# Optimization experiments

Hardware: AMD Instinct MI355X
Metric: run time of the kernel (lower is better)

The kernel has to match this reference:

```python
import jax, jax.numpy as jnp
import numpy as np


def _conv(x, w, b):
    # 3x3 stride-1 pad-1 conv, NCHW / OIHW
    y = jax.lax.conv_general_dilated(x, w, (1, 1), 'SAME',
                                     dimension_numbers=('NCHW', 'OIHW', 'NCHW'))
    return y + b[None, :, None, None]


def _lrelu(x):
    return jax.nn.leaky_relu(x, negative_slope=0.2)


def setup_inputs() -> dict:
    key = jax.random.key(0)
    ks = jax.random.split(key, 12)
    B, H, W = 64, 32, 32
    C, K, DH, OUT = 16, 10, 256, 784

    def w(k, shape, fan_in):
        return jax.random.normal(k, shape, jnp.float32) / np.sqrt(fan_in)

    inp = {
        'x':   jax.random.normal(ks[0], (B, 1, H, W), jnp.float32),
        # encoder convs
        'cw1': w(ks[1], (C, 1, 3, 3), 1 * 9),   'cb1': jnp.zeros((C,), jnp.float32),
        'cw2': w(ks[2], (C, C, 3, 3), C * 9),   'cb2': jnp.zeros((C,), jnp.float32),
        # 2 residual blocks, 2 convs each
        'r1w1': w(ks[3], (C, C, 3, 3), C * 9), 'r1b1': jnp.zeros((C,), jnp.float32),
        'r1w2': w(ks[4], (C, C, 3, 3), C * 9), 'r1b2': jnp.zeros((C,), jnp.float32),
        'r2w1': w(ks[5], (C, C, 3, 3), C * 9), 'r2b1': jnp.zeros((C,), jnp.float32),
        'r2w2': w(ks[6], (C, C, 3, 3), C * 9), 'r2b2': jnp.zeros((C,), jnp.float32),
        # VQ codebook (k=10 hardcoded in source, d = encoder channels)
        'codebook': jax.random.normal(ks[7], (K, C), jnp.float32),
        # decoder MLP 16 -> 256 -> 256 -> 784 (torch Linear layout: [out, in])
        'dw1': w(ks[8], (DH, C), C),     'db1': jnp.zeros((DH,), jnp.float32),
        'dw2': w(ks[9], (DH, DH), DH),   'db2': jnp.zeros((DH,), jnp.float32),
        'dw3': w(ks[10], (OUT, DH), DH), 'db3': jnp.zeros((OUT,), jnp.float32),
    }
    return inp


def reference(x, cw1, cb1, cw2, cb2,
              r1w1, r1b1, r1w2, r1b2, r2w1, r2b1, r2w2, r2b2,
              codebook, dw1, db1, dw2, db2, dw3, db3):
    # ---- encoder ----
    h = _lrelu(_conv(x, cw1, cb1))
    h = _lrelu(_conv(h, cw2, cb2))
    h = _lrelu(_conv(_lrelu(_conv(h, r1w1, r1b1)), r1w2, r1b2)) + h  # ResBlock 1
    h = _lrelu(_conv(_lrelu(_conv(h, r2w1, r2b1)), r2w2, r2b2)) + h  # ResBlock 2
    z_e = h  # [B, C, H, W]

    # ---- VQ: cdist^2 + argmin + gather ----
    B, C, H, W = z_e.shape
    x_flat = z_e.transpose(0, 2, 3, 1).reshape(-1, C)          # [N, C]
    d2 = (jnp.sum(x_flat ** 2, axis=1, keepdims=True)
          + jnp.sum(codebook ** 2, axis=1)[None, :]
          - 2.0 * x_flat @ codebook.T)                          # [N, K]
    idx = jnp.argmin(d2, axis=1)                                # [N]
    z_q = codebook[idx].reshape(B, H, W, C).transpose(0, 3, 1, 2)
    # straight-through (as written in source: value == z_e, grad flows via z_q)
    z_st = z_q + jax.lax.stop_gradient(z_e - z_q)               # [B, C, H, W]

    # ---- decoder: per-pixel MLP 16 -> 256 -> 256 -> 784 ----
    g = z_st.transpose(0, 2, 3, 1)                              # [B, H, W, C]
    g = _lrelu(g @ dw1.T + db1)
    g = _lrelu(g @ dw2.T + db2)
    x_recon = jax.nn.sigmoid(g @ dw3.T + db3)                   # [B, H, W, 784]
    return x_recon, z_e, z_st, z_q
```

## Files before the change

kernel.cpp:

```cpp
#include <hip/hip_runtime.h>

typedef __attribute__((ext_vector_type(8))) short bfrag;
typedef __attribute__((ext_vector_type(4))) float ffrag;

__device__ __forceinline__ float lrelu(float x) { return x > 0.f ? x : 0.2f * x; }

__device__ __forceinline__ short f2b(float f) {
    union { float f; unsigned u; } x; x.f = f;
    unsigned r = x.u + 0x7fffu + ((x.u >> 16) & 1u);
    return (short)(r >> 16);
}

__global__ __launch_bounds__(256) void prep_k(
    const float* __restrict__ dw1, const float* __restrict__ dw2, const float* __restrict__ dw3,
    short* __restrict__ dw1p, short* __restrict__ dw2b, short* __restrict__ dw3b)
{
    const int i = blockIdx.x * 256 + threadIdx.x;
    if (i < 65536)  dw2b[i] = f2b(dw2[i]);
    if (i < 200704) dw3b[i] = f2b(dw3[i]);
    if (i < 8192) {
        const int row = i >> 5, k = i & 31;
        dw1p[i] = (k < 16) ? f2b(dw1[row * 16 + k]) : (short)0;
    }
}

template<int CIN, bool RES, bool VQ>
__global__ __launch_bounds__(256, 6) void conv3_k(
    const float* __restrict__ in, const float* __restrict__ wgt,
    const float* __restrict__ bias, const float* __restrict__ res,
    float* __restrict__ out,
    const float* __restrict__ cbk, float* __restrict__ zq,
    float* __restrict__ zst, short* __restrict__ zstb)
{
    __shared__ float sw[16 * CIN * 9];
    __shared__ float si[CIN][4][34];
    __shared__ float sx[VQ ? 64 * 17 : 1];
    __shared__ float scb[VQ ? 160 : 1];
    __shared__ int   sbest[VQ ? 64 : 1];

    const int t = threadIdx.x;
    const int b = blockIdx.x >> 4;
    const int band = blockIdx.x & 15;
    const float* ip = in + (size_t)b * CIN * 1024;

    for (int i = t; i < 16 * CIN * 9; i += 256) sw[i] = wgt[i];
    if (VQ) { if (t < 160) scb[t] = cbk[t]; }
    for (int i = t; i < CIN * 136; i += 256) {
        const int ci = i / 136;
        const int rem = i - ci * 136;
        const int rr = rem / 34;
        const int cc = rem - rr * 34;
        const int row = band * 2 + rr - 1;
        const int cv  = cc - 1;
        si[ci][rr][cc] = (row >= 0 && row < 32 && cv >= 0 && cv < 32)
                       ? ip[ci * 1024 + row * 32 + cv] : 0.f;
    }
    __syncthreads();

    const int w0 = (t & 15) * 2;
    const int rr = (t >> 4) & 1;
    const int co = (t >> 5) * 2;

    float acc[2][2];
    #pragma unroll
    for (int j = 0; j < 2; ++j) {
        const float bv = bias[co + j];
        acc[j][0] = bv; acc[j][1] = bv;
    }

    #pragma unroll
    for (int ci = 0; ci < CIN; ++ci)
        #pragma unroll
        for (int kh = 0; kh < 3; ++kh) {
            const float* srow = &si[ci][rr + kh][w0];
            float v[4];
            #pragma unroll
            for (int m = 0; m < 4; ++m) v[m] = srow[m];
            #pragma unroll
            for (int j = 0; j < 2; ++j) {
                const float* wp = &sw[((co + j) * CIN + ci) * 9 + kh * 3];
                #pragma unroll
                for (int kw = 0; kw < 3; ++kw) {
                    const float wv = wp[kw];
                    acc[j][0] = fmaf(v[kw],     wv, acc[j][0]);
                    acc[j][1] = fmaf(v[kw + 1], wv, acc[j][1]);
                }
            }
        }

    const int row = band * 2 + rr;
    #pragma unroll
    for (int j = 0; j < 2; ++j) {
        const size_t o = (size_t)b * 16384 + (size_t)(co + j) * 1024 + row * 32 + w0;
        float2 ov;
        ov.x = lrelu(acc[j][0]); ov.y = lrelu(acc[j][1]);
        if (RES) {
            const float2 rv = *(const float2*)&res[o];
            ov.x += rv.x; ov.y += rv.y;
        }
        *(float2*)&out[o] = ov;
        if (VQ) {
            sx[(rr * 32 + w0)     * 17 + co + j] = ov.x;
            sx[(rr * 32 + w0 + 1) * 17 + co + j] = ov.y;
        }
    }

    if (VQ) {
        __syncthreads();
        if (t < 64) {
            float x[16]; float xx = 0.f;
            #pragma unroll
            for (int c = 0; c < 16; ++c) { x[c] = sx[t * 17 + c]; xx += x[c] * x[c]; }
            int best = 0; float bestd = 1e30f;
            #pragma unroll
            for (int k = 0; k < 10; ++k) {
                float dot = 0.f, cn = 0.f;
                #pragma unroll
                for (int c = 0; c < 16; ++c) { const float cv = scb[k * 16 + c]; dot += x[c] * cv; cn += cv * cv; }
                const float d2 = xx + cn - 2.f * dot;
                if (d2 < bestd) { bestd = d2; best = k; }
            }
            sbest[t] = best;
            unsigned pk[8];
            #pragma unroll
            for (int c = 0; c < 16; ++c) {
                const float q = scb[best * 16 + c];
                const float s = q + (x[c] - q);
                const unsigned hb = (unsigned)(unsigned short)f2b(s);
                if (c & 1) pk[c >> 1] |= hb << 16; else pk[c >> 1] = hb;
            }
            const size_t n = (size_t)b * 1024 + (band * 2 + (t >> 5)) * 32 + (t & 31);
            uint4* d = (uint4*)(zstb + n * 16);
            d[0] = make_uint4(pk[0], pk[1], pk[2], pk[3]);
            d[1] = make_uint4(pk[4], pk[5], pk[6], pk[7]);
        }
        __syncthreads();
        for (int i = t; i < 1024; i += 256) {
            const int c  = i >> 6;
            const int rw = i & 63;
            const float q = scb[sbest[rw] * 16 + c];
            const float x = sx[rw * 17 + c];
            const size_t a = (size_t)b * 16384 + (size_t)c * 1024 + band * 64 + rw;
            zq[a]  = q;
            zst[a] = q + (x - q);
        }
    }
}

__global__ __launch_bounds__(256, 2) void decoder_k(
    const short* __restrict__ zstb,
    const short* __restrict__ dw1p, const float* __restrict__ db1,
    const short* __restrict__ dw2b, const float* __restrict__ db2,
    const short* __restrict__ dw3b, const float* __restrict__ db3,
    float* __restrict__ xrec)
{
    __shared__ short g[4 * 8192];
    __shared__ short b3[2][4096];

    const int t    = threadIdx.x;
    const int lane = t & 63;
    const int wid  = t >> 6;
    const int lr   = lane & 15;
    const int lg   = lane >> 4;
    const int row0 = blockIdx.x * 128 + wid * 32;
    short* gw = g + wid * 8192;

    #define GB(row, kbyte) (((row) * 512 + (kbyte)) ^ (((row) & 7) << 4))

    auto stage2 = [&](short* dst, const short* src) {
        #pragma unroll
        for (int h = 0; h < 2; ++h) {
            const int L = h * 4096 + t * 16;
            const int S = L ^ (((L >> 9) & 7) << 4);
            __builtin_amdgcn_global_load_lds(
                (const __attribute__((address_space(1))) void*)((const char*)src + S),
                (__attribute__((address_space(3))) void*)((char*)dst + L), 16, 0, 0);
        }
    };

    stage2(&b3[0][0], dw2b);

    {
        bfrag A1[2];
        #pragma unroll
        for (int rt = 0; rt < 2; ++rt) {
            bfrag z;
            #pragma unroll
            for (int i = 0; i < 8; ++i) z[i] = 0;
            if (lg < 2)
                z = *(const bfrag*)&zstb[(size_t)(row0 + rt * 16 + lr) * 16 + lg * 8];
            A1[rt] = z;
        }
        #pragma unroll
        for (int ct = 0; ct < 16; ++ct) {
            const int col = ct * 16 + lr;
            const bfrag B = *(const bfrag*)&dw1p[col * 32 + lg * 8];
            const float bv = db1[col];
            ffrag acc[2];
            #pragma unroll
            for (int rt = 0; rt < 2; ++rt) {
                #pragma unroll
                for (int q = 0; q < 4; ++q) acc[rt][q] = bv;
                acc[rt] = __builtin_amdgcn_mfma_f32_16x16x32_bf16(A1[rt], B, acc[rt], 0, 0, 0);
            }
            #pragma unroll
            for (int rt = 0; rt < 2; ++rt)
                #pragma unroll
                for (int q = 0; q < 4; ++q) {
                    const int R = rt * 16 + lg * 4 + q;
                    *(short*)((char*)gw + GB(R, col * 2)) = f2b(lrelu(acc[rt][q]));
                }
        }
    }

    bfrag A[2][8];
    #pragma unroll
    for (int rt = 0; rt < 2; ++rt)
        #pragma unroll
        for (int kk = 0; kk < 8; ++kk)
            A[rt][kk] = *(const bfrag*)((char*)gw + GB(rt * 16 + lr, kk * 64 + lg * 16));

    __syncthreads();

    #pragma unroll 1
    for (int p = 0; p < 16; ++p) {
        if (p < 15) stage2(&b3[(p + 1) & 1][0], dw2b + (p + 1) * 4096);
        else        stage2(&b3[0][0],           dw3b);
        const char* bp = (const char*)&b3[p & 1][0];
        const int col = p * 16 + lr;
        bfrag Bf[8];
        #pragma unroll
        for (int kk = 0; kk < 8; ++kk)
            Bf[kk] = *(const bfrag*)(bp + (((lr * 512 + kk * 64 + lg * 16)) ^ ((lr & 7) << 4)));
        ffrag aE[2], aO[2];
        const float bv = db2[col];
        #pragma unroll
        for (int rt = 0; rt < 2; ++rt)
            #pragma unroll
            for (int q = 0; q < 4; ++q) { aE[rt][q] = bv; aO[rt][q] = 0.f; }
        #pragma unroll
        for (int kk = 0; kk < 8; kk += 2)
            #pragma unroll
            for (int rt = 0; rt < 2; ++rt) {
                aE[rt] = __builtin_amdgcn_mfma_f32_16x16x32_bf16(A[rt][kk],     Bf[kk],     aE[rt], 0, 0, 0);
                aO[rt] = __builtin_amdgcn_mfma_f32_16x16x32_bf16(A[rt][kk + 1], Bf[kk + 1], aO[rt], 0, 0, 0);
            }
        #pragma unroll
        for (int rt = 0; rt < 2; ++rt)
            #pragma unroll
            for (int q = 0; q < 4; ++q) {
                const int R = rt * 16 + lg * 4 + q;
                *(short*)((char*)gw + GB(R, col * 2)) = f2b(lrelu(aE[rt][q] + aO[rt][q]));
            }
        __syncthreads();
    }

    #pragma unroll
    for (int rt = 0; rt < 2; ++rt)
        #pragma unroll
        for (int kk = 0; kk < 8; ++kk)
            A[rt][kk] = *(const bfrag*)((char*)gw + GB(rt * 16 + lr, kk * 64 + lg * 16));

    float* slab = (float*)gw;

    #pragma unroll 1
    for (int p = 0; p < 49; ++p) {
        if (p < 48) stage2(&b3[(p + 1) & 1][0], dw3b + (p + 1) * 4096);
        const char* bp = (const char*)&b3[p & 1][0];
        const int col = p * 16 + lr;
        bfrag Bf[8];
        #pragma unroll
        for (int kk = 0; kk < 8; ++kk)
            Bf[kk] = *(const bfrag*)(bp + (((lr * 512 + kk * 64 + lg * 16)) ^ ((lr & 7) << 4)));
        ffrag aE[2], aO[2];
        const float bv = db3[col];
        #pragma unroll
        for (int rt = 0; rt < 2; ++rt)
            #pragma unroll
            for (int q = 0; q < 4; ++q) { aE[rt][q] = bv; aO[rt][q] = 0.f; }
        #pragma unroll
        for (int kk = 0; kk < 8; kk += 2)
            #pragma unroll
            for (int rt = 0; rt < 2; ++rt) {
                aE[rt] = __builtin_amdgcn_mfma_f32_16x16x32_bf16(A[rt][kk],     Bf[kk],     aE[rt], 0, 0, 0);
                aO[rt] = __builtin_amdgcn_mfma_f32_16x16x32_bf16(A[rt][kk + 1], Bf[kk + 1], aO[rt], 0, 0, 0);
            }
        const int ph = p & 1;
        #pragma unroll
        for (int rt = 0; rt < 2; ++rt)
            #pragma unroll
            for (int q = 0; q < 4; ++q) {
                const int R = rt * 16 + lg * 4 + q;
                const float v = aE[rt][q] + aO[rt][q];
                slab[R * 36 + ph * 16 + lr] = 1.f / (1.f + __expf(-v));
            }
        if (ph) {
            const int cb = (p - 1) * 16;
            #pragma unroll
            for (int f0 = 0; f0 < 4; ++f0) {
                const int f = f0 * 64 + lane;
                const int row = f >> 3, c4 = f & 7;
                const float4 v = *(const float4*)&slab[row * 36 + c4 * 4];
                *(float4*)&xrec[(size_t)(row0 + row) * 784 + cb + c4 * 4] = v;
            }
        }
        if (p == 48) {
            #pragma unroll
            for (int f0 = 0; f0 < 2; ++f0) {
                const int f = f0 * 64 + lane;
                const int row = f >> 2, c4 = f & 3;
                const float4 v = *(const float4*)&slab[row * 36 + c4 * 4];
                *(float4*)&xrec[(size_t)(row0 + row) * 784 + 768 + c4 * 4] = v;
            }
        }
        __syncthreads();
    }
    #undef GB
}

extern "C" void kernel_launch(void* const* d_in, const int* in_sizes, int n_in,
                              void* d_out, int out_size, void* d_ws, size_t ws_size,
                              hipStream_t stream) {
    const float* x    = (const float*)d_in[0];
    const float* cw1  = (const float*)d_in[1];
    const float* cb1  = (const float*)d_in[2];
    const float* cw2  = (const float*)d_in[3];
    const float* cb2  = (const float*)d_in[4];
    const float* r1w1 = (const float*)d_in[5];
    const float* r1b1 = (const float*)d_in[6];
    const float* r1w2 = (const float*)d_in[7];
    const float* r1b2 = (const float*)d_in[8];
    const float* r2w1 = (const float*)d_in[9];
    const float* r2b1 = (const float*)d_in[10];
    const float* r2w2 = (const float*)d_in[11];
    const float* r2b2 = (const float*)d_in[12];
    const float* cbk  = (const float*)d_in[13];
    const float* dw1  = (const float*)d_in[14];
    const float* db1  = (const float*)d_in[15];
    const float* dw2  = (const float*)d_in[16];
    const float* db2  = (const float*)d_in[17];
    const float* dw3  = (const float*)d_in[18];
    const float* db3  = (const float*)d_in[19];

    float* out  = (float*)d_out;
    float* xrec = out;
    float* ze   = out + 51380224;
    float* zst  = ze + 1048576;
    float* zq   = zst + 1048576;

    float* A  = (float*)d_ws;
    float* Bf = A + (1 << 20);
    float* Cf = Bf + (1 << 20);
    short* wsb  = (short*)(Cf + (1 << 20));
    short* zstb = wsb;
    short* dw2b = zstb + 1048576;
    short* dw3b = dw2b + 65536;
    short* dw1p = dw3b + 200704;

    prep_k<<<784, 256, 0, stream>>>(dw1, dw2, dw3, dw1p, dw2b, dw3b);

    conv3_k<1,  false, false><<<1024, 256, 0, stream>>>(x,  cw1,  cb1,  nullptr, A,  nullptr, nullptr, nullptr, nullptr);
    conv3_k<16, false, false><<<1024, 256, 0, stream>>>(A,  cw2,  cb2,  nullptr, Bf, nullptr, nullptr, nullptr, nullptr);
    conv3_k<16, false, false><<<1024, 256, 0, stream>>>(Bf, r1w1, r1b1, nullptr, Cf, nullptr, nullptr, nullptr, nullptr);
    conv3_k<16, true,  false><<<1024, 256, 0, stream>>>(Cf, r1w2, r1b2, Bf, A,  nullptr, nullptr, nullptr, nullptr);
    conv3_k<16, false, false><<<1024, 256, 0, stream>>>(A,  r2w1, r2b1, nullptr, Cf, nullptr, nullptr, nullptr, nullptr);
    conv3_k<16, true,  true ><<<1024, 256, 0, stream>>>(Cf, r2w2, r2b2, A, ze, cbk, zq, zst, zstb);

    decoder_k<<<512, 256, 0, stream>>>(zstb, dw1p, db1, dw2b, db2, dw3b, db3, xrec);
}
```

Baseline: 169.0 us.

## Fuse six encoder convs and VQ into one halo-tiled kernel

```diff
diff --git a/kernel.cpp b/kernel.cpp
--- a/kernel.cpp
+++ b/kernel.cpp
@@ -13,7 +13,11 @@
 
 __global__ __launch_bounds__(256) void prep_k(
     const float* __restrict__ dw1, const float* __restrict__ dw2, const float* __restrict__ dw3,
-    short* __restrict__ dw1p, short* __restrict__ dw2b, short* __restrict__ dw3b)
+    const float* __restrict__ cw1, const float* __restrict__ cw2,
+    const float* __restrict__ r1w1, const float* __restrict__ r1w2,
+    const float* __restrict__ r2w1, const float* __restrict__ r2w2,
+    short* __restrict__ dw1p, short* __restrict__ dw2b, short* __restrict__ dw3b,
+    float* __restrict__ wtr)
 {
     const int i = blockIdx.x * 256 + threadIdx.x;
     if (i < 65536)  dw2b[i] = f2b(dw2[i]);
@@ -22,128 +26,153 @@
         const int row = i >> 5, k = i & 31;
         dw1p[i] = (k < 16) ? f2b(dw1[row * 16 + k]) : (short)0;
     }
-}
-
-template<int CIN, bool RES, bool VQ>
-__global__ __launch_bounds__(256, 6) void conv3_k(
-    const float* __restrict__ in, const float* __restrict__ wgt,
-    const float* __restrict__ bias, const float* __restrict__ res,
-    float* __restrict__ out,
-    const float* __restrict__ cbk, float* __restrict__ zq,
+    if (i < 2304) {
+        const int co = i & 15;
+        const int q  = i >> 4;
+        const int k  = q % 9;
+        const int ci = q / 9;
+        const int src = (co * 16 + ci) * 9 + k;
+        wtr[2304 * 1 + i] = cw2 [src];
+        wtr[2304 * 2 + i] = r1w1[src];
+        wtr[2304 * 3 + i] = r1w2[src];
+        wtr[2304 * 4 + i] = r2w1[src];
+        wtr[2304 * 5 + i] = r2w2[src];
+        if (ci == 0) wtr[i] = cw1[co * 9 + k];
+    }
+}
+
+template<int CIN, int RIN, int ROUT, int HOUT, bool HASRES, int RRES, int HRES>
+__device__ __forceinline__ void conv_stage(
+    const float* __restrict__ in, float* __restrict__ out, const float* __restrict__ res,
+    const float* __restrict__ wt, const float* __restrict__ bias, int r0, int t)
+{
+    const int lo = (r0 - HOUT > 0) ? r0 - HOUT : 0;
+    const int hi = (r0 + 8 + HOUT < 32) ? r0 + 8 + HOUT : 32;
+    const int base = r0 - HOUT;
+    const int nlow = lo - base;
+    const int hih  = hi - base;
+    if (nlow > 0 || hih < ROUT) {
+        const int nz = (nlow + (ROUT - hih)) * 36;
+        for (int i = t; i < 16 * nz; i += 512) {
+            const int ch = i / nz, rem = i % nz;
+            int r = rem / 36; const int c = rem % 36;
+            r = (r < nlow) ? r : (hih + (r - nlow));
+            out[(ch * ROUT + r) * 36 + c] = 0.f;
+        }
+    }
+    for (int i = t; i < 16 * ROUT * 2; i += 512) {
+        const int ch = i / (ROUT * 2), rem = i % (ROUT * 2);
+        out[(ch * ROUT + (rem >> 1)) * 36 + ((rem & 1) ? 33 : 0)] = 0.f;
+    }
+
+    const int n = (hi - lo) * 32;
+    for (int u = t; u < n; u += 512) {
+        const int row = lo + (u >> 5), col = u & 31;
+        const int prin = row - r0 + HOUT;
+        float acc[16];
+        #pragma unroll
+        for (int co = 0; co < 16; ++co) acc[co] = bias[co];
+        for (int ci = 0; ci < CIN; ++ci) {
+            const float* ip = in + (ci * RIN + prin) * 36 + col;
+            float v[9];
+            #pragma unroll
+            for (int kh = 0; kh < 3; ++kh)
+                #pragma unroll
+                for (int kw = 0; kw < 3; ++kw) v[kh * 3 + kw] = ip[kh * 36 + kw];
+            const float* wp = wt + ci * 144;
+            #pragma unroll
+            for (int k = 0; k < 9; ++k)
+                #pragma unroll
+                for (int co = 0; co < 16; ++co)
+                    acc[co] = fmaf(v[k], wp[k * 16 + co], acc[co]);
+        }
+        const int pro = row - base;
+        #pragma unroll
+        for (int co = 0; co < 16; ++co) {
+            float val = lrelu(acc[co]);
+            if (HASRES) val += res[(co * RRES + (row - (r0 - HRES))) * 36 + col + 1];
+            out[(co * ROUT + pro) * 36 + col + 1] = val;
+        }
+    }
+    __syncthreads();
+}
+
+__global__ __launch_bounds__(512, 1) void enc_k(
+    const float* __restrict__ x, const float* __restrict__ wtr,
+    const float* __restrict__ cb1, const float* __restrict__ cb2,
+    const float* __restrict__ r1b1, const float* __restrict__ r1b2,
+    const float* __restrict__ r2b1, const float* __restrict__ r2b2,
+    const float* __restrict__ cbk,
+    float* __restrict__ ze, float* __restrict__ zq,
     float* __restrict__ zst, short* __restrict__ zstb)
 {
-    __shared__ float sw[16 * CIN * 9];
-    __shared__ float si[CIN][4][34];
-    __shared__ float sx[VQ ? 64 * 17 : 1];
-    __shared__ float scb[VQ ? 160 : 1];
-    __shared__ int   sbest[VQ ? 64 : 1];
-
-    const int t = threadIdx.x;
-    const int b = blockIdx.x >> 4;
-    const int band = blockIdx.x & 15;
-    const float* ip = in + (size_t)b * CIN * 1024;
-
-    for (int i = t; i < 16 * CIN * 9; i += 256) sw[i] = wgt[i];
-    if (VQ) { if (t < 160) scb[t] = cbk[t]; }
-    for (int i = t; i < CIN * 136; i += 256) {
-        const int ci = i / 136;
-        const int rem = i - ci * 136;
-        const int rr = rem / 34;
-        const int cc = rem - rr * 34;
-        const int row = band * 2 + rr - 1;
-        const int cv  = cc - 1;
-        si[ci][rr][cc] = (row >= 0 && row < 32 && cv >= 0 && cv < 32)
-                       ? ip[ci * 1024 + row * 32 + cv] : 0.f;
+    __shared__ float xb[20 * 36];
+    __shared__ float Abuf[16 * 18 * 36];
+    __shared__ float Bbuf[16 * 16 * 36];
+    __shared__ float Cbuf[16 * 12 * 36];
+    __shared__ float scb[160];
+    __shared__ int   sbest[256];
+
+    const int t  = threadIdx.x;
+    const int b  = blockIdx.x >> 2;
+    const int r0 = (blockIdx.x & 3) * 8;
+
+    if (t < 160) scb[t] = cbk[t];
+    for (int i = t; i < 720; i += 512) {
+        const int r = i / 36, c = i % 36;
+        const int rl = r0 - 6 + r, cl = c - 1;
+        xb[i] = (rl >= 0 && rl < 32 && cl >= 0 && cl < 32)
+              ? x[(size_t)b * 1024 + rl * 32 + cl] : 0.f;
     }
     __syncthreads();
 
-    const int w0 = (t & 15) * 2;
-    const int rr = (t >> 4) & 1;
-    const int co = (t >> 5) * 2;
-
-    float acc[2][2];
-    #pragma unroll
-    for (int j = 0; j < 2; ++j) {
-        const float bv = bias[co + j];
-        acc[j][0] = bv; acc[j][1] = bv;
-    }
-
-    #pragma unroll
-    for (int ci = 0; ci < CIN; ++ci)
-        #pragma unroll
-        for (int kh = 0; kh < 3; ++kh) {
-            const float* srow = &si[ci][rr + kh][w0];
-            float v[4];
-            #pragma unroll
-            for (int m = 0; m < 4; ++m) v[m] = srow[m];
-            #pragma unroll
-            for (int j = 0; j < 2; ++j) {
-                const float* wp = &sw[((co + j) * CIN + ci) * 9 + kh * 3];
-                #pragma unroll
-                for (int kw = 0; kw < 3; ++kw) {
-                    const float wv = wp[kw];
-                    acc[j][0] = fmaf(v[kw],     wv, acc[j][0]);
-                    acc[j][1] = fmaf(v[kw + 1], wv, acc[j][1]);
-                }
-            }
-        }
-
-    const int row = band * 2 + rr;
-    #pragma unroll
-    for (int j = 0; j < 2; ++j) {
-        const size_t o = (size_t)b * 16384 + (size_t)(co + j) * 1024 + row * 32 + w0;
-        float2 ov;
-        ov.x = lrelu(acc[j][0]); ov.y = lrelu(acc[j][1]);
-        if (RES) {
-            const float2 rv = *(const float2*)&res[o];
-            ov.x += rv.x; ov.y += rv.y;
-        }
-        *(float2*)&out[o] = ov;
-        if (VQ) {
-            sx[(rr * 32 + w0)     * 17 + co + j] = ov.x;
-            sx[(rr * 32 + w0 + 1) * 17 + co + j] = ov.y;
-        }
-    }
-
-    if (VQ) {
-        __syncthreads();
-        if (t < 64) {
-            float x[16]; float xx = 0.f;
-            #pragma unroll
-            for (int c = 0; c < 16; ++c) { x[c] = sx[t * 17 + c]; xx += x[c] * x[c]; }
-            int best = 0; float bestd = 1e30f;
-            #pragma unroll
-            for (int k = 0; k < 10; ++k) {
-                float dot = 0.f, cn = 0.f;
-                #pragma unroll
-                for (int c = 0; c < 16; ++c) { const float cv = scb[k * 16 + c]; dot += x[c] * cv; cn += cv * cv; }
-                const float d2 = xx + cn - 2.f * dot;
-                if (d2 < bestd) { bestd = d2; best = k; }
-            }
-            sbest[t] = best;
-            unsigned pk[8];
-            #pragma unroll
-            for (int c = 0; c < 16; ++c) {
-                const float q = scb[best * 16 + c];
-                const float s = q + (x[c] - q);
-                const unsigned hb = (unsigned)(unsigned short)f2b(s);
-                if (c & 1) pk[c >> 1] |= hb << 16; else pk[c >> 1] = hb;
-            }
-            const size_t n = (size_t)b * 1024 + (band * 2 + (t >> 5)) * 32 + (t & 31);
-            uint4* d = (uint4*)(zstb + n * 16);
-            d[0] = make_uint4(pk[0], pk[1], pk[2], pk[3]);
-            d[1] = make_uint4(pk[4], pk[5], pk[6], pk[7]);
-        }
-        __syncthreads();
-        for (int i = t; i < 1024; i += 256) {
-            const int c  = i >> 6;
-            const int rw = i & 63;
-            const float q = scb[sbest[rw] * 16 + c];
-            const float x = sx[rw * 17 + c];
-            const size_t a = (size_t)b * 16384 + (size_t)c * 1024 + band * 64 + rw;
-            zq[a]  = q;
-            zst[a] = q + (x - q);
-        }
+    conv_stage<1,  20, 18, 5, false,  1, 0>(xb,   Abuf, nullptr, wtr,          cb1,  r0, t);
+    conv_stage<16, 18, 16, 4, false,  1, 0>(Abuf, Bbuf, nullptr, wtr + 2304,   cb2,  r0, t);
+    conv_stage<16, 16, 14, 3, false,  1, 0>(Bbuf, Abuf, nullptr, wtr + 4608,   r1b1, r0, t);
+    conv_stage<16, 14, 12, 2, true,  16, 4>(Abuf, Cbuf, Bbuf,    wtr + 6912,   r1b2, r0, t);
+    conv_stage<16, 12, 10, 1, false,  1, 0>(Cbuf, Abuf, nullptr, wtr + 9216,   r2b1, r0, t);
+    conv_stage<16, 10,  8, 0, true,  12, 2>(Abuf, Bbuf, Cbuf,    wtr + 11520,  r2b2, r0, t);
+
+    const size_t obase = (size_t)b * 16384 + r0 * 32;
+    for (int i = t; i < 4096; i += 512) {
+        const int c = i >> 8, px = i & 255;
+        ze[obase + c * 1024 + px] = Bbuf[(c * 8 + (px >> 5)) * 36 + (px & 31) + 1];
+    }
+    if (t < 256) {
+        const int r = t >> 5, col = t & 31;
+        float xv[16]; float xx = 0.f;
+        #pragma unroll
+        for (int c = 0; c < 16; ++c) { xv[c] = Bbuf[(c * 8 + r) * 36 + col + 1]; xx += xv[c] * xv[c]; }
+        int best = 0; float bestd = 1e30f;
+        #pragma unroll
+        for (int k = 0; k < 10; ++k) {
+            float dot = 0.f, cn = 0.f;
+            #pragma unroll
+            for (int c = 0; c < 16; ++c) { const float cv = scb[k * 16 + c]; dot += xv[c] * cv; cn += cv * cv; }
+            const float d2 = xx + cn - 2.f * dot;
+            if (d2 < bestd) { bestd = d2; best = k; }
+        }
+        sbest[t] = best;
+        unsigned pk[8];
+        #pragma unroll
+        for (int c = 0; c < 16; ++c) {
+            const float q = scb[best * 16 + c];
+            const float s = q + (xv[c] - q);
+            const unsigned hb = (unsigned)(unsigned short)f2b(s);
+            if (c & 1) pk[c >> 1] |= hb << 16; else pk[c >> 1] = hb;
+        }
+        const size_t n = (size_t)b * 1024 + (size_t)(r0 + r) * 32 + col;
+        uint4* d = (uint4*)(zstb + n * 16);
+        d[0] = make_uint4(pk[0], pk[1], pk[2], pk[3]);
+        d[1] = make_uint4(pk[4], pk[5], pk[6], pk[7]);
+    }
+    __syncthreads();
+    for (int i = t; i < 4096; i += 512) {
+        const int c = i >> 8, px = i & 255;
+        const float q  = scb[sbest[px] * 16 + c];
+        const float xv = Bbuf[(c * 8 + (px >> 5)) * 36 + (px & 31) + 1];
+        zq[obase + c * 1024 + px]  = q;
+        zst[obase + c * 1024 + px] = q + (xv - q);
     }
 }
 
@@ -348,23 +377,17 @@
     float* zst  = ze + 1048576;
     float* zq   = zst + 1048576;
 
-    float* A  = (float*)d_ws;
-    float* Bf = A + (1 << 20);
-    float* Cf = Bf + (1 << 20);
-    short* wsb  = (short*)(Cf + (1 << 20));
-    short* zstb = wsb;
+    short* zstb = (short*)d_ws;
     short* dw2b = zstb + 1048576;
     short* dw3b = dw2b + 65536;
     short* dw1p = dw3b + 200704;
-
-    prep_k<<<784, 256, 0, stream>>>(dw1, dw2, dw3, dw1p, dw2b, dw3b);
-
-    conv3_k<1,  false, false><<<1024, 256, 0, stream>>>(x,  cw1,  cb1,  nullptr, A,  nullptr, nullptr, nullptr, nullptr);
-    conv3_k<16, false, false><<<1024, 256, 0, stream>>>(A,  cw2,  cb2,  nullptr, Bf, nullptr, nullptr, nullptr, nullptr);
-    conv3_k<16, false, false><<<1024, 256, 0, stream>>>(Bf, r1w1, r1b1, nullptr, Cf, nullptr, nullptr, nullptr, nullptr);
-    conv3_k<16, true,  false><<<1024, 256, 0, stream>>>(Cf, r1w2, r1b2, Bf, A,  nullptr, nullptr, nullptr, nullptr);
-    conv3_k<16, false, false><<<1024, 256, 0, stream>>>(A,  r2w1, r2b1, nullptr, Cf, nullptr, nullptr, nullptr, nullptr);
-    conv3_k<16, true,  true ><<<1024, 256, 0, stream>>>(Cf, r2w2, r2b2, A, ze, cbk, zq, zst, zstb);
+    float* wtr  = (float*)(dw1p + 8192);
+
+    prep_k<<<784, 256, 0, stream>>>(dw1, dw2, dw3, cw1, cw2, r1w1, r1w2, r2w1, r2w2,
+                                    dw1p, dw2b, dw3b, wtr);
+
+    enc_k<<<256, 512, 0, stream>>>(x, wtr, cb1, cb2, r1b1, r1b2, r2b1, r2b2,
+                                   cbk, ze, zq, zst, zstb);
 
     decoder_k<<<512, 256, 0, stream>>>(zstb, dw1p, db1, dw2b, db2, dw3b, db3, xrec);
 }
```

Measured after the change: 156.0 us. 1.08x faster.
